# Performance work log

Hardware: AMD Instinct MI355X
Metric: run time of the kernel (lower is better)

Reference implementation:

```python
import jax, jax.numpy as jnp
import numpy as np

# Memristor nonideality constants (from disturbed_outputs_i_v_non_linear)
G_MIN = 1e-4
G_MAX = 5e-4
K_V = 1.05
V_REF = jnp.array([-1.2, -0.9, -0.6, -0.3, 0.0, 0.3, 0.6, 0.9, 1.2], dtype=jnp.float32)
G_REF = jnp.array([0.0, 1e-4, 3e-4, 5e-4], dtype=jnp.float32)
I_REF = jnp.array([
    [0, 0, 0, 0, 0, 0, 0, 0, 0],
    [-1.5e-4, -1.1e-4, -7e-5, -3e-5, 0, 3e-5, 7e-5, 1.1e-4, 1.5e-4],
    [-5e-4, -3.5e-4, -2.2e-4, -9e-5, 0, 9e-5, 2.2e-4, 3.5e-4, 5e-4],
    [-9e-4, -6e-4, -3.7e-4, -1.5e-4, 0, 1.5e-4, 3.7e-4, 6e-4, 9e-4],
], dtype=jnp.float32)


def setup_inputs() -> dict:
    key = jax.random.key(0)
    k1, k2, k3 = jax.random.split(key, 3)
    n_in, n_out, batch = 1024, 1024, 128
    stdv = 1.0 / np.sqrt(n_in)
    x = jax.random.uniform(k1, (batch, n_in), dtype=jnp.float32)  # pixel-like inputs in [0,1]
    w = jax.random.normal(k2, (n_in, n_out), dtype=jnp.float32) * stdv  # RandomNormal(stddev=1/sqrt(n_in))
    b = jax.random.normal(k3, (n_out,), dtype=jnp.float32) * 0.01
    return {"x": x, "w": w, "b": b}


def reference(x, w, b):
    """Faithful jax port of memristor_dense.call: augment input with ones column,
    stack bias under weights, then nonlinear memristor I-V crossbar product."""
    B = x.shape[0]
    weights = jnp.concatenate([w, b[None, :]], axis=0)              # [N1, M], N1 = n_in+1
    inputs = jnp.concatenate([x, jnp.ones((B, 1), x.dtype)], axis=1)  # [B, N1]
    N1, M = weights.shape

    # w -> effective conductance (differential-pair effective mapping)
    max_weight = jnp.max(jnp.abs(weights))
    k_G = (G_MAX - G_MIN) / max_weight
    G_eff = k_G * weights                                            # [N1, M], signed
    V = K_V * inputs                                                 # [B, N1]

    # 1) interpolate reference I-V curve along V for each conductance level
    #    (jnp.interp clamps outside the V_REF grid, matching lookup-table behavior)
    I_at_V = jax.vmap(lambda Ir: jnp.interp(V, V_REF, Ir))(I_REF)    # [L, B, N1]

    # 2) linear interpolation along G on |G_eff| (odd symmetry in G via sign)
    Gabs = jnp.abs(G_eff)                                            # [N1, M]
    L = G_REF.shape[0]
    idx = jnp.clip(jnp.searchsorted(G_REF, Gabs, side='right') - 1, 0, L - 2)  # [N1, M]
    g0 = G_REF[idx]
    g1 = G_REF[idx + 1]
    t = ((Gabs - g0) / (g1 - g0))[:, :, None]                        # [N1, M, 1]

    jidx = jnp.arange(N1)[:, None]                                   # [N1, 1] broadcasts with idx
    I_lo = I_at_V[idx, :, jidx]                                      # [N1, M, B]
    I_hi = I_at_V[idx + 1, :, jidx]                                  # [N1, M, B]
    sgn = jnp.sign(G_eff)[:, :, None]
    I_ind = sgn * ((1.0 - t) * I_lo + t * I_hi)                      # per-device currents [N1, M, B]

    I_total = jnp.sum(I_ind, axis=0).T                               # [B, M]

    # current -> output: y = I / (k_V * k_G); reduces to x @ W for an ideal linear device
    y = I_total / (K_V * k_G)
    return y
```

## Files before the change

### kernel.cpp

```cpp
#include <hip/hip_runtime.h>
#include <hip/hip_bf16.h>
#include <cstdint>

#define K_V_C   1.05f
#define G_DIFF  4.0e-4f
#define KP4     4608

typedef __attribute__((ext_vector_type(8))) short short8;
typedef __attribute__((ext_vector_type(4))) float f32x4;

__device__ __constant__ float c_I1[9] = {-0.00015f,-0.00011f,-7e-05f,-3e-05f,0.f,3e-05f,7e-05f,0.00011f,0.00015f};
__device__ __constant__ float c_I2[9] = {-0.0005f,-0.00035f,-0.00022f,-9e-05f,0.f,9e-05f,0.00022f,0.00035f,0.0005f};
__device__ __constant__ float c_I3[9] = {-0.0009f,-0.0006f,-0.00037f,-0.00015f,0.f,0.00015f,0.00037f,0.0006f,0.0009f};

__device__ inline unsigned short f2bf(float f) {
  unsigned int u = __float_as_uint(f);
  u += 0x7FFFu + ((u >> 16) & 1u);
  return (unsigned short)(u >> 16);
}

__device__ inline void interp3(float v, float& u1, float& u2, float& u3) {
  const float sf = v * 3.3333333333333335f + 4.0f;
  float fs = floorf(sf);
  fs = fminf(fmaxf(fs, 0.f), 7.f);
  const int   s  = (int)fs;
  const float fr = fminf(fmaxf(sf - fs, 0.f), 1.f);
  u1 = fmaf(fr, c_I1[s+1] - c_I1[s], c_I1[s]);
  u2 = fmaf(fr, c_I2[s+1] - c_I2[s], c_I2[s]);
  u3 = fmaf(fr, c_I3[s+1] - c_I3[s], c_I3[s]);
}

__device__ inline void coeff3f(float g, float& c1, float& c2, float& c3) {
  const float    ga = fabsf(g);
  const unsigned sb = __float_as_uint(g) & 0x80000000u;
  const float t1 = fminf(ga * 1e4f, 1.f);
  const float t2 = fminf(fmaxf((ga - 1e-4f) * 5e3f, 0.f), 1.f);
  const float t3 = fmaxf((ga - 3e-4f) * 5e3f, 0.f);
  c1 = __uint_as_float(__float_as_uint(t1 - t2) | sb);
  c2 = __uint_as_float(__float_as_uint(t2 - t3) | sb);
  c3 = __uint_as_float(__float_as_uint(t3) | sb);
}

__device__ inline void coeff3(float g, float& c1, float& c2, float& c3) {
  const float ga  = fabsf(g);
  const float sgn = (g > 0.f) ? 1.f : ((g < 0.f) ? -1.f : 0.f);
  const int   idx = (ga >= 3e-4f) ? 2 : ((ga >= 1e-4f) ? 1 : 0);
  const float g0   = (idx == 0) ? 0.f : ((idx == 1) ? 1e-4f : 3e-4f);
  const float invd = (idx == 0) ? 1e4f : 5e3f;
  const float t    = (ga - g0) * invd;
  const float clo = sgn * (1.f - t), chi = sgn * t;
  c1 = (idx == 0) ? chi : ((idx == 1) ? clo : 0.f);
  c2 = (idx == 1) ? chi : ((idx == 2) ? clo : 0.f);
  c3 = (idx == 2) ? chi : 0.f;
}

__global__ __launch_bounds__(256) void prep1_kernel(
    const float* __restrict__ x, const float* __restrict__ w,
    const float* __restrict__ bias, float* __restrict__ partials,
    unsigned short* __restrict__ Ub) {
  const int t = threadIdx.x, bid = blockIdx.x;
  if (bid < 1024) {
    const int i = bid * 256 + t;
    const float4 v = ((const float4*)w)[i];
    float m = fmaxf(fmaxf(fabsf(v.x), fabsf(v.y)), fmaxf(fabsf(v.z), fabsf(v.w)));
    if (i < 256) {
      const float4 bv = ((const float4*)bias)[i];
      m = fmaxf(m, fmaxf(fmaxf(fabsf(bv.x), fabsf(bv.y)),
                         fmaxf(fabsf(bv.z), fabsf(bv.w))));
    }
    #pragma unroll
    for (int o = 32; o > 0; o >>= 1) m = fmaxf(m, __shfl_down(m, o, 64));
    __shared__ float red[4];
    if ((t & 63) == 0) red[t >> 6] = m;
    __syncthreads();
    if (t == 0)
      partials[bid] = fmaxf(fmaxf(red[0], red[1]), fmaxf(red[2], red[3]));
  } else {
    const int idx = (bid - 1024) * 256 + t;
    const int b = idx / 288, j4 = idx - b * 288;
    ushort4 o0 = make_ushort4(0,0,0,0), o1 = o0, o2 = o0, o3 = o0;
    if (j4 < 256) {
      const float4 xv = ((const float4*)x)[b * 256 + j4];
      float u1, u2, u3;
      interp3(K_V_C * xv.x, u1, u2, u3); o0 = make_ushort4(f2bf(u1), f2bf(u2), f2bf(u3), 0);
      interp3(K_V_C * xv.y, u1, u2, u3); o1 = make_ushort4(f2bf(u1), f2bf(u2), f2bf(u3), 0);
      interp3(K_V_C * xv.z, u1, u2, u3); o2 = make_ushort4(f2bf(u1), f2bf(u2), f2bf(u3), 0);
      interp3(K_V_C * xv.w, u1, u2, u3); o3 = make_ushort4(f2bf(u1), f2bf(u2), f2bf(u3), 0);
    } else if (j4 == 256) {
      float u1, u2, u3;
      interp3(K_V_C, u1, u2, u3);
      o0 = make_ushort4(f2bf(u1), f2bf(u2), f2bf(u3), 0);
    }
    ushort4* dst = (ushort4*)(Ub + (size_t)b * KP4 + j4 * 16);
    dst[0] = o0; dst[1] = o1; dst[2] = o2; dst[3] = o3;
  }
}

__global__ __launch_bounds__(512, 8) void fusedgemm_kernel(
    const float* __restrict__ w, const float* __restrict__ bias,
    const float* __restrict__ partials, const unsigned short* __restrict__ Ub,
    float* __restrict__ out) {
  __shared__ __align__(16) unsigned short panel[18432];
  const int t = threadIdx.x;
  const int wv = t >> 6, lane = t & 63, la = lane & 15, kg = lane >> 4;
  const int b0 = (blockIdx.x >> 6) * 16;
  const int n0 = (blockIdx.x & 63) * 16;

  #pragma unroll
  for (int i = 0; i < 8; ++i) {
    const int idx = i * 512 + t;
    const int row = idx >> 2, c4 = idx & 3;
    const float4 v = *(const float4*)(w + (size_t)row * 1024 + n0 + c4 * 4);
    panel[row * 16 + c4 * 4 + 0] = f2bf(v.x);
    panel[row * 16 + c4 * 4 + 1] = f2bf(v.y);
    panel[row * 16 + c4 * 4 + 2] = f2bf(v.z);
    panel[row * 16 + c4 * 4 + 3] = f2bf(v.w);
  }
  if (t < 16) panel[1024 * 16 + t] = f2bf(bias[n0 + t]);
  for (int i = 1025 * 16 + t; i < 1152 * 16; i += 512) panel[i] = 0;

  float mx = 0.f;
  #pragma unroll
  for (int i = 0; i < 4; ++i) {
    const float4 p = ((const float4*)partials)[lane + i * 64];
    mx = fmaxf(mx, fmaxf(fmaxf(p.x, p.y), fmaxf(p.z, p.w)));
  }
  #pragma unroll
  for (int o = 1; o < 64; o <<= 1) mx = fmaxf(mx, __shfl_xor(mx, o, 64));
  const float maxw = mx;
  const float kG   = G_DIFF / maxw;
  __syncthreads();

  const unsigned short* Ap = Ub + (size_t)(b0 + la) * KP4 + wv * 576 + kg * 8;
  const int jb = wv * 144 + kg * 2;
  f32x4 acc = {0.f, 0.f, 0.f, 0.f};
  #pragma unroll 6
  for (int ks = 0; ks < 18; ++ks) {
    const short8 a = *(const short8*)(Ap + ks * 32);
    const int j0 = jb + ks * 8;
    const float wa = __uint_as_float((unsigned)panel[j0 * 16 + la] << 16);
    const float wb = __uint_as_float((unsigned)panel[(j0 + 1) * 16 + la] << 16);
    float a1, a2, a3, b1, b2, b3;
    coeff3f(kG * wa, a1, a2, a3);
    coeff3f(kG * wb, b1, b2, b3);
    union { __hip_bfloat162 h[4]; short8 s; } bf;
    bf.h[0] = __float22bfloat162_rn(make_float2(a1, a2));
    bf.h[1] = __float22bfloat162_rn(make_float2(a3, 0.f));
    bf.h[2] = __float22bfloat162_rn(make_float2(b1, b2));
    bf.h[3] = __float22bfloat162_rn(make_float2(b3, 0.f));
    acc = __builtin_amdgcn_mfma_f32_16x16x32_bf16(a, bf.s, acc, 0, 0, 0);
  }

  float* P = (float*)panel;
  __syncthreads();
  *(float4*)&P[wv * 256 + lane * 4] = make_float4(acc[0], acc[1], acc[2], acc[3]);
  __syncthreads();
  if (t < 256) {
    float s = 0.f;
    #pragma unroll
    for (int ww = 0; ww < 8; ++ww) s += P[ww * 256 + t];
    const int l2 = t >> 2, ai = t & 3;
    const int row = b0 + ((l2 >> 4) << 2) + ai;
    const int col = n0 + (l2 & 15);
    out[(size_t)row * 1024 + col] = s * (maxw * (1.0f / (K_V_C * G_DIFF)));
  }
}

__global__ __launch_bounds__(256) void maxabs_atomic_kernel(
    const float* __restrict__ w, const float* __restrict__ b,
    unsigned int* __restrict__ wsmax) {
  const int NW4 = 262144, NB4 = 256;
  float m = 0.f;
  for (int i = blockIdx.x * blockDim.x + threadIdx.x; i < NW4 + NB4;
       i += gridDim.x * blockDim.x) {
    float4 v = (i < NW4) ? ((const float4*)w)[i] : ((const float4*)b)[i - NW4];
    m = fmaxf(m, fmaxf(fmaxf(fabsf(v.x), fabsf(v.y)),
                       fmaxf(fabsf(v.z), fabsf(v.w))));
  }
  #pragma unroll
  for (int o = 32; o > 0; o >>= 1) m = fmaxf(m, __shfl_down(m, o, 64));
  __shared__ float red[4];
  if ((threadIdx.x & 63) == 0) red[threadIdx.x >> 6] = m;
  __syncthreads();
  if (threadIdx.x == 0)
    atomicMax(wsmax, __float_as_uint(fmaxf(fmaxf(red[0], red[1]),
                                           fmaxf(red[2], red[3]))));
}

__global__ __launch_bounds__(256) void memristor_atomic_kernel(
    const float* __restrict__ x, const float* __restrict__ w,
    const float* __restrict__ bias, const unsigned int* __restrict__ wsmax,
    float* __restrict__ out) {
  __shared__ float4 U[2048];
  const int tid = threadIdx.x;
  const float maxw  = __uint_as_float(*wsmax);
  const float kG    = G_DIFF / maxw;
  const float scale = maxw * (1.0f / (K_V_C * G_DIFF));
  const int mq = tid & 15, bg = tid >> 4;
  const int m0 = blockIdx.x * 64 + mq * 4;
  const int swz = bg & 7;
  float acc[4][8];
  #pragma unroll
  for (int a = 0; a < 4; ++a)
    #pragma unroll
    for (int c = 0; c < 8; ++c) acc[a][c] = 0.f;
  for (int sc = blockIdx.y; sc < 65; sc += 16) {
    const int j0 = sc * 16;
    const int nj = min(16, 1025 - j0);
    __syncthreads();
    #pragma unroll
    for (int k = 0; k < 8; ++k) {
      const int e = k * 256 + tid;
      const int jl = e & 15, b = e >> 4;
      const int jg = j0 + jl;
      if (jg <= 1024) {
        const float v = (jg < 1024) ? K_V_C * x[b * 1024 + jg] : K_V_C;
        float u1, u2, u3;
        interp3(v, u1, u2, u3);
        U[b * 16 + (jl ^ ((b >> 3) & 7))] = make_float4(0.f, u1, u2, u3);
      }
    }
    __syncthreads();
    for (int jl = 0; jl < nj; ++jl) {
      const int jg = j0 + jl;
      const float4 wv = (jg < 1024) ? *(const float4*)(w + jg * 1024 + m0)
                                    : *(const float4*)(bias + m0);
      const float warr[4] = {wv.x, wv.y, wv.z, wv.w};
      float c1[4], c2[4], c3[4];
      #pragma unroll
      for (int mi = 0; mi < 4; ++mi) coeff3(kG * warr[mi], c1[mi], c2[mi], c3[mi]);
      const int base = bg * 128 + (jl ^ swz);
      #pragma unroll
      for (int bb = 0; bb < 8; ++bb) {
        const float4 u = U[base + bb * 16];
        #pragma unroll
        for (int mi = 0; mi < 4; ++mi)
          acc[mi][bb] = fmaf(c1[mi], u.y, fmaf(c2[mi], u.z, fmaf(c3[mi], u.w, acc[mi][bb])));
      }
    }
  }
  #pragma unroll
  for (int bb = 0; bb < 8; ++bb) {
    const int b = bg * 8 + bb;
    #pragma unroll
    for (int mi = 0; mi < 4; ++mi)
      atomicAdd(&out[b * 1024 + m0 + mi], acc[mi][bb] * scale);
  }
}

extern "C" void kernel_launch(void* const* d_in, const int* in_sizes, int n_in,
                              void* d_out, int out_size, void* d_ws, size_t ws_size,
                              hipStream_t stream) {
  const float* x = (const float*)d_in[0];
  const float* w = (const float*)d_in[1];
  const float* b = (const float*)d_in[2];
  float* out = (float*)d_out;

  float*          partials = (float*)((char*)d_ws + 128);
  unsigned short* Ub = (unsigned short*)((char*)d_ws + 8192);
  const size_t need = 8192 + (size_t)128 * KP4 * 2;

  if (ws_size >= need) {
    prep1_kernel<<<1168, 256, 0, stream>>>(x, w, b, partials, Ub);
    fusedgemm_kernel<<<512, 512, 0, stream>>>(w, b, partials, Ub, out);
  } else {
    unsigned int* wsmax = (unsigned int*)d_ws;
    hipMemsetAsync(wsmax, 0, 4, stream);
    maxabs_atomic_kernel<<<256, 256, 0, stream>>>(w, b, wsmax);
    hipMemsetAsync(out, 0, (size_t)out_size * sizeof(float), stream);
    dim3 grid(16, 16);
    memristor_atomic_kernel<<<grid, 256, 0, stream>>>(x, w, b, wsmax, out);
  }
}
```

Before: 21.88 us.

## Widen fused GEMM tile to 32 columns with 1024-thread blocks, two MFMA accumulators

Each block now covers a 16x32 output tile instead of 16x16, using 16 waves that each handle half as many K steps. Every loaded A fragment feeds two MFMAs, which halves the global reads of the interpolated input per output column and halves the grid to 256 blocks. Panel stores also become vectorised ushort4 writes. In exchange, shared memory per block doubles and the cross-wave reduction grows to 16 partials, while the smaller grid may leave some compute units underused.

```diff
diff --git a/kernel.cpp b/kernel.cpp
--- a/kernel.cpp
+++ b/kernel.cpp
@@ -17,6 +17,10 @@
   unsigned int u = __float_as_uint(f);
   u += 0x7FFFu + ((u >> 16) & 1u);
   return (unsigned short)(u >> 16);
+}
+
+__device__ inline float bf2f(unsigned short h) {
+  return __uint_as_float((unsigned int)h << 16);
 }
 
 __device__ inline void interp3(float v, float& u1, float& u2, float& u3) {
@@ -96,28 +100,26 @@
   }
 }
 
-__global__ __launch_bounds__(512, 8) void fusedgemm_kernel(
+__global__ __launch_bounds__(1024, 4) void fusedgemm_kernel(
     const float* __restrict__ w, const float* __restrict__ bias,
     const float* __restrict__ partials, const unsigned short* __restrict__ Ub,
     float* __restrict__ out) {
-  __shared__ __align__(16) unsigned short panel[18432];
+  __shared__ __align__(16) unsigned short panel[36864];
   const int t = threadIdx.x;
   const int wv = t >> 6, lane = t & 63, la = lane & 15, kg = lane >> 4;
-  const int b0 = (blockIdx.x >> 6) * 16;
-  const int n0 = (blockIdx.x & 63) * 16;
+  const int b0 = (blockIdx.x >> 5) * 16;
+  const int n0 = (blockIdx.x & 31) * 32;
 
   #pragma unroll
   for (int i = 0; i < 8; ++i) {
-    const int idx = i * 512 + t;
-    const int row = idx >> 2, c4 = idx & 3;
+    const int idx = i * 1024 + t;
+    const int row = idx >> 3, c4 = idx & 7;
     const float4 v = *(const float4*)(w + (size_t)row * 1024 + n0 + c4 * 4);
-    panel[row * 16 + c4 * 4 + 0] = f2bf(v.x);
-    panel[row * 16 + c4 * 4 + 1] = f2bf(v.y);
-    panel[row * 16 + c4 * 4 + 2] = f2bf(v.z);
-    panel[row * 16 + c4 * 4 + 3] = f2bf(v.w);
-  }
-  if (t < 16) panel[1024 * 16 + t] = f2bf(bias[n0 + t]);
-  for (int i = 1025 * 16 + t; i < 1152 * 16; i += 512) panel[i] = 0;
+    *(ushort4*)&panel[row * 32 + c4 * 4] =
+        make_ushort4(f2bf(v.x), f2bf(v.y), f2bf(v.z), f2bf(v.w));
+  }
+  if (t < 32) panel[1024 * 32 + t] = f2bf(bias[n0 + t]);
+  for (int i = 1025 * 32 + t; i < 1152 * 32; i += 1024) panel[i] = 0;
 
   float mx = 0.f;
   #pragma unroll
@@ -131,37 +133,49 @@
   const float kG   = G_DIFF / maxw;
   __syncthreads();
 
-  const unsigned short* Ap = Ub + (size_t)(b0 + la) * KP4 + wv * 576 + kg * 8;
-  const int jb = wv * 144 + kg * 2;
-  f32x4 acc = {0.f, 0.f, 0.f, 0.f};
-  #pragma unroll 6
-  for (int ks = 0; ks < 18; ++ks) {
+  const unsigned short* Ap = Ub + (size_t)(b0 + la) * KP4 + wv * 288 + kg * 8;
+  const int jb = wv * 72 + kg * 2;
+  f32x4 acc0 = {0.f, 0.f, 0.f, 0.f};
+  f32x4 acc1 = {0.f, 0.f, 0.f, 0.f};
+  #pragma unroll 3
+  for (int ks = 0; ks < 9; ++ks) {
     const short8 a = *(const short8*)(Ap + ks * 32);
     const int j0 = jb + ks * 8;
-    const float wa = __uint_as_float((unsigned)panel[j0 * 16 + la] << 16);
-    const float wb = __uint_as_float((unsigned)panel[(j0 + 1) * 16 + la] << 16);
-    float a1, a2, a3, b1, b2, b3;
-    coeff3f(kG * wa, a1, a2, a3);
-    coeff3f(kG * wb, b1, b2, b3);
-    union { __hip_bfloat162 h[4]; short8 s; } bf;
-    bf.h[0] = __float22bfloat162_rn(make_float2(a1, a2));
-    bf.h[1] = __float22bfloat162_rn(make_float2(a3, 0.f));
-    bf.h[2] = __float22bfloat162_rn(make_float2(b1, b2));
-    bf.h[3] = __float22bfloat162_rn(make_float2(b3, 0.f));
-    acc = __builtin_amdgcn_mfma_f32_16x16x32_bf16(a, bf.s, acc, 0, 0, 0);
+    const float w0a = bf2f(panel[j0 * 32 + la]);
+    const float w0b = bf2f(panel[(j0 + 1) * 32 + la]);
+    const float w1a = bf2f(panel[j0 * 32 + 16 + la]);
+    const float w1b = bf2f(panel[(j0 + 1) * 32 + 16 + la]);
+    float a1, a2, a3, b1, b2, b3, c1, c2, c3, d1, d2, d3;
+    coeff3f(kG * w0a, a1, a2, a3);
+    coeff3f(kG * w0b, b1, b2, b3);
+    coeff3f(kG * w1a, c1, c2, c3);
+    coeff3f(kG * w1b, d1, d2, d3);
+    union { __hip_bfloat162 h[4]; short8 s; } bf0, bf1;
+    bf0.h[0] = __float22bfloat162_rn(make_float2(a1, a2));
+    bf0.h[1] = __float22bfloat162_rn(make_float2(a3, 0.f));
+    bf0.h[2] = __float22bfloat162_rn(make_float2(b1, b2));
+    bf0.h[3] = __float22bfloat162_rn(make_float2(b3, 0.f));
+    bf1.h[0] = __float22bfloat162_rn(make_float2(c1, c2));
+    bf1.h[1] = __float22bfloat162_rn(make_float2(c3, 0.f));
+    bf1.h[2] = __float22bfloat162_rn(make_float2(d1, d2));
+    bf1.h[3] = __float22bfloat162_rn(make_float2(d3, 0.f));
+    acc0 = __builtin_amdgcn_mfma_f32_16x16x32_bf16(a, bf0.s, acc0, 0, 0, 0);
+    acc1 = __builtin_amdgcn_mfma_f32_16x16x32_bf16(a, bf1.s, acc1, 0, 0, 0);
   }
 
   float* P = (float*)panel;
   __syncthreads();
-  *(float4*)&P[wv * 256 + lane * 4] = make_float4(acc[0], acc[1], acc[2], acc[3]);
-  __syncthreads();
-  if (t < 256) {
+  *(float4*)&P[wv * 512 + lane * 4]       = make_float4(acc0[0], acc0[1], acc0[2], acc0[3]);
+  *(float4*)&P[wv * 512 + 256 + lane * 4] = make_float4(acc1[0], acc1[1], acc1[2], acc1[3]);
+  __syncthreads();
+  if (t < 512) {
     float s = 0.f;
     #pragma unroll
-    for (int ww = 0; ww < 8; ++ww) s += P[ww * 256 + t];
-    const int l2 = t >> 2, ai = t & 3;
+    for (int ww = 0; ww < 16; ++ww) s += P[ww * 512 + t];
+    const int frag = t >> 8, f = t & 255;
+    const int l2 = f >> 2, ai = f & 3;
     const int row = b0 + ((l2 >> 4) << 2) + ai;
-    const int col = n0 + (l2 & 15);
+    const int col = n0 + frag * 16 + (l2 & 15);
     out[(size_t)row * 1024 + col] = s * (maxw * (1.0f / (K_V_C * G_DIFF)));
   }
 }
@@ -262,7 +276,7 @@
 
   if (ws_size >= need) {
     prep1_kernel<<<1168, 256, 0, stream>>>(x, w, b, partials, Ub);
-    fusedgemm_kernel<<<512, 512, 0, stream>>>(w, b, partials, Ub, out);
+    fusedgemm_kernel<<<256, 1024, 0, stream>>>(w, b, partials, Ub, out);
   } else {
     unsigned int* wsmax = (unsigned int*)d_ws;
     hipMemsetAsync(wsmax, 0, 4, stream);
```

After: 18.30 us, median of 2. 16.4% less time.
